# Kernel optimization log

Hardware: AMD Instinct MI355X
Metric: run time of the kernel (lower is better)

The kernel has to match this reference:

```python
import jax, jax.numpy as jnp
import numpy as np
import math

BSZ, SEQ, DM = 2, 2048, 2048
NH, NKV, HD = 16, 8, 128
INTER = 8192
THETA = 10000.0
EPS = 1e-6
SOFTCAP = 50.0


def quant_per_token(x):
    # dynamic per-token symmetric int8 quant: scale = max|x|/127
    s = jnp.max(jnp.abs(x), axis=-1, keepdims=True) / 127.0
    s = jnp.maximum(s, 1e-8)
    q = jnp.clip(jnp.round(x / s), -127.0, 127.0)
    return q, s


def quant_weight(w):
    # per-output-channel symmetric int8 quant (rows are out channels)
    s = jnp.max(jnp.abs(w), axis=1, keepdims=True) / 127.0
    q = jnp.clip(jnp.round(w / s), -127.0, 127.0)
    return q, s


def w8a8_linear(qx, sx, w):
    # int8 GEMM with fused dequant: (qx @ qw^T) * s_act * s_weight
    qw, sw = quant_weight(w)
    return (qx @ qw.T) * sx * sw.T


def rmsnorm_quant(x, w):
    # RMSNormGeneral: w * x / sqrt(mean(x^2)+eps), then per-token quant
    var = jnp.mean(x * x, axis=-1, keepdims=True)
    y = x * jax.lax.rsqrt(var + EPS) * w
    return quant_per_token(y)


def rope_tables(seqlen, dim, theta):
    inv_freq = 1.0 / theta ** (jnp.arange(0, dim, 2, dtype=jnp.float32) / dim)
    pos = jnp.arange(seqlen, dtype=jnp.float32)
    fh = pos[:, None] * inv_freq[None, :]            # [S, dim/2]
    freqs = jnp.concatenate([fh, fh], axis=-1)       # [S, dim]
    return jnp.cos(freqs), jnp.sin(freqs)


def apply_rope(x, cos, sin):
    # x: [B, S, H, D]; rotate-half RoPE
    d2 = x.shape[-1] // 2
    rot = jnp.concatenate([-x[..., d2:], x[..., :d2]], axis=-1)
    return x * cos[None, :, None, :] + rot * sin[None, :, None, :]


def attention(q, k, v, mask, softcap):
    # q: [B, NH, S, D]; k, v: [B, NKV, S, D]
    groups = q.shape[1] // k.shape[1]
    if groups > 1:
        k = jnp.repeat(k, groups, axis=1)
        v = jnp.repeat(v, groups, axis=1)
    scores = jnp.einsum('bhqd,bhkd->bhqk', q, k) / math.sqrt(q.shape[-1])
    if softcap:
        scores = jnp.tanh(scores / softcap) * softcap
    scores = scores + mask
    attn = jax.nn.softmax(scores, axis=-1)
    out = jnp.einsum('bhqk,bhkd->bhqd', attn, v)
    return out.transpose(0, 2, 1, 3).reshape(q.shape[0], q.shape[2], -1)


def setup_inputs() -> dict:
    key = jax.random.key(0)
    ks = jax.random.split(key, 7)
    return {
        'hidden_states': jax.random.normal(ks[0], (BSZ, SEQ, DM), jnp.float32),
        'w_in_norm': jax.random.normal(ks[1], (DM,), jnp.float32) * 0.1 + 1.0,
        'w_post_norm': jax.random.normal(ks[2], (DM,), jnp.float32) * 0.1 + 1.0,
        'wqkv': jax.random.normal(ks[3], (NH * HD + 2 * NKV * HD, DM), jnp.float32) * 0.02,
        'wo': jax.random.normal(ks[4], (DM, NH * HD), jnp.float32) * 0.02,
        'w_gate_up': jax.random.normal(ks[5], (2 * INTER, DM), jnp.float32) * 0.02,
        'w_down': jax.random.normal(ks[6], (DM, INTER), jnp.float32) * 0.02,
    }


def reference(hidden_states, w_in_norm, w_post_norm, wqkv, wo, w_gate_up, w_down):
    q_dim, kv_dim = NH * HD, NKV * HD
    T = BSZ * SEQ
    x = hidden_states.reshape(T, DM)

    # --- attention block ---
    residual = x
    qx, sx = rmsnorm_quant(x, w_in_norm)
    qkv = w8a8_linear(qx, sx, wqkv)                      # [T, q_dim+2*kv_dim]
    q, k, v = jnp.split(qkv, [q_dim, q_dim + kv_dim], axis=-1)
    q = q.reshape(BSZ, SEQ, NH, HD)
    k = k.reshape(BSZ, SEQ, NKV, HD)
    v = v.reshape(BSZ, SEQ, NKV, HD).transpose(0, 2, 1, 3)

    cos, sin = rope_tables(SEQ, HD, THETA)
    q = apply_rope(q, cos, sin).transpose(0, 2, 1, 3)    # [B, NH, S, D]
    k = apply_rope(k, cos, sin).transpose(0, 2, 1, 3)    # [B, NKV, S, D]

    causal = jnp.tril(jnp.ones((SEQ, SEQ), dtype=bool))
    mask = jnp.where(causal, 0.0, -1e9).astype(jnp.float32)[None, None]
    attn_out = attention(q, k, v, mask, SOFTCAP).reshape(T, q_dim)

    qa, sa = quant_per_token(attn_out)
    x = residual + w8a8_linear(qa, sa, wo)

    # --- MLP block ---
    residual = x
    qx, sx = rmsnorm_quant(x, w_post_norm)
    gateup = w8a8_linear(qx, sx, w_gate_up)              # [T, 2*INTER]
    gate, up = jnp.split(gateup, 2, axis=-1)
    act = jax.nn.gelu(gate, approximate=True) * up       # gelu_and_mul
    qm, sm = quant_per_token(act)
    x = residual + w8a8_linear(qm, sm, w_down)

    return x.reshape(BSZ, SEQ, DM)
```

## Files before the change

kernel.cpp:

```cpp
#include <hip/hip_runtime.h>
#include <cstdint>
#include <math.h>

#define T_TOKENS 4096
#define SEQ 2048
#define DM 2048
#define NH 16
#define NKV 8
#define HD 128
#define QDIM 2048
#define KVDIM 1024
#define QKVN 4096
#define INTER 8192
#define GUN 16384

typedef int v4i __attribute__((ext_vector_type(4)));
typedef float v4f __attribute__((ext_vector_type(4)));
typedef short s8v __attribute__((ext_vector_type(8)));
typedef short s4v __attribute__((ext_vector_type(4)));
typedef short s2v __attribute__((ext_vector_type(2)));

#define GL16(g, l)                                                                       \
  __builtin_amdgcn_global_load_lds((__attribute__((address_space(1))) const void*)(g),   \
                                   (__attribute__((address_space(3))) void*)(l), 16, 0, 0)

__device__ inline float wave_sum(float v) {
#pragma unroll
  for (int off = 32; off > 0; off >>= 1) v += __shfl_down(v, off);
  return v;
}
__device__ inline float wave_max(float v) {
#pragma unroll
  for (int off = 32; off > 0; off >>= 1) v = fmaxf(v, __shfl_down(v, off));
  return v;
}
__device__ inline float dot4(float4 a, float4 b) {
  return a.x * b.x + a.y * b.y + a.z * b.z + a.w * b.w;
}
__device__ inline int8_t quant1(float v, float s) {
  float q = rintf(v / s);
  q = fminf(fmaxf(q, -127.f), 127.f);
  return (int8_t)(int)q;
}
__device__ inline unsigned short f2bf_rne(float x) {
  unsigned u = __float_as_uint(x);
  return (unsigned short)((u + 0x7FFFu + ((u >> 16) & 1u)) >> 16);
}
__device__ inline float bf2f(unsigned short h) { return __uint_as_float(((unsigned)h) << 16); }

__global__ void rope_table_kernel(float* __restrict__ cosT, float* __restrict__ sinT) {
  int s = blockIdx.x, d = threadIdx.x;
  float inv = 1.0f / powf(10000.0f, (float)d * (1.0f / 64.0f));
  float f = (float)s * inv;
  cosT[s * 64 + d] = cosf(f);
  sinT[s * 64 + d] = sinf(f);
}

__global__ __launch_bounds__(256) void quant_w_kernel(const float* __restrict__ w,
                                                      int8_t* __restrict__ qw,
                                                      float* __restrict__ sw, int K) {
  __shared__ float red[4];
  int row = blockIdx.x, tid = threadIdx.x;
  const float* wr = w + (size_t)row * K;
  int nv = K >> 10;
  float4 v[8];
  float mx = 0.f;
#pragma unroll
  for (int i = 0; i < 8; i++) {
    if (i < nv) {
      v[i] = *(const float4*)(wr + (size_t)(tid + i * 256) * 4);
      mx = fmaxf(mx, fmaxf(fmaxf(fabsf(v[i].x), fabsf(v[i].y)),
                           fmaxf(fabsf(v[i].z), fabsf(v[i].w))));
    }
  }
  mx = wave_max(mx);
  if ((tid & 63) == 0) red[tid >> 6] = mx;
  __syncthreads();
  float m = fmaxf(fmaxf(red[0], red[1]), fmaxf(red[2], red[3]));
  float s = m * (1.0f / 127.0f);
  if (tid == 0) sw[row] = s;
  float sd = (s > 0.f) ? s : 1.f;
  int8_t* qr = qw + (size_t)row * K;
#pragma unroll
  for (int i = 0; i < 8; i++) {
    if (i < nv) {
      char4 o;
      o.x = quant1(v[i].x, sd);
      o.y = quant1(v[i].y, sd);
      o.z = quant1(v[i].z, sd);
      o.w = quant1(v[i].w, sd);
      *(char4*)(qr + (size_t)(tid + i * 256) * 4) = o;
    }
  }
}

__global__ __launch_bounds__(256) void quant_w_gu_kernel(const float* __restrict__ w,
                                                         int8_t* __restrict__ qw,
                                                         float* __restrict__ sw) {
  __shared__ float red[4];
  int row = blockIdx.x, tid = threadIdx.x;
  const int K = DM;
  int j = (row < INTER) ? row : row - INTER;
  int pr = (j >> 6) * 128 + ((j >> 4) & 3) * 32 + ((row < INTER) ? 0 : 16) + (j & 15);
  const float* wr = w + (size_t)row * K;
  float4 v[2];
  float mx = 0.f;
#pragma unroll
  for (int i = 0; i < 2; i++) {
    v[i] = *(const float4*)(wr + (size_t)(tid + i * 256) * 4);
    mx = fmaxf(mx, fmaxf(fmaxf(fabsf(v[i].x), fabsf(v[i].y)),
                         fmaxf(fabsf(v[i].z), fabsf(v[i].w))));
  }
  mx = wave_max(mx);
  if ((tid & 63) == 0) red[tid >> 6] = mx;
  __syncthreads();
  float m = fmaxf(fmaxf(red[0], red[1]), fmaxf(red[2], red[3]));
  float s = m * (1.0f / 127.0f);
  if (tid == 0) sw[pr] = s;
  float sd = (s > 0.f) ? s : 1.f;
  int8_t* qr = qw + (size_t)pr * K;
#pragma unroll
  for (int i = 0; i < 2; i++) {
    char4 o;
    o.x = quant1(v[i].x, sd);
    o.y = quant1(v[i].y, sd);
    o.z = quant1(v[i].z, sd);
    o.w = quant1(v[i].w, sd);
    *(char4*)(qr + (size_t)(tid + i * 256) * 4) = o;
  }
}

__global__ __launch_bounds__(256) void rmsnorm_quant_kernel(const float* __restrict__ x,
                                                            const float* __restrict__ w,
                                                            int8_t* __restrict__ q,
                                                            float* __restrict__ s) {
  __shared__ float red[8];
  int t = blockIdx.x, tid = threadIdx.x;
  const float* xr = x + (size_t)t * DM;
  float4 a = *(const float4*)(xr + tid * 8);
  float4 b = *(const float4*)(xr + tid * 8 + 4);
  float ss = dot4(a, a) + dot4(b, b);
  ss = wave_sum(ss);
  if ((tid & 63) == 0) red[tid >> 6] = ss;
  __syncthreads();
  float tot = red[0] + red[1] + red[2] + red[3];
  float rms = rsqrtf(tot * (1.0f / DM) + 1e-6f);
  float4 wa = *(const float4*)(w + tid * 8);
  float4 wb = *(const float4*)(w + tid * 8 + 4);
  float y[8] = {a.x * rms * wa.x, a.y * rms * wa.y, a.z * rms * wa.z, a.w * rms * wa.w,
                b.x * rms * wb.x, b.y * rms * wb.y, b.z * rms * wb.z, b.w * rms * wb.w};
  float mx = 0.f;
#pragma unroll
  for (int i = 0; i < 8; i++) mx = fmaxf(mx, fabsf(y[i]));
  mx = wave_max(mx);
  if ((tid & 63) == 0) red[4 + (tid >> 6)] = mx;
  __syncthreads();
  float m = fmaxf(fmaxf(red[4], red[5]), fmaxf(red[6], red[7]));
  float sc = fmaxf(m * (1.0f / 127.0f), 1e-8f);
  if (tid == 0) s[t] = sc;
  int8_t* qr = q + (size_t)t * DM + tid * 8;
  char4 o0, o1;
  o0.x = quant1(y[0], sc); o0.y = quant1(y[1], sc); o0.z = quant1(y[2], sc); o0.w = quant1(y[3], sc);
  o1.x = quant1(y[4], sc); o1.y = quant1(y[5], sc); o1.z = quant1(y[6], sc); o1.w = quant1(y[7], sc);
  *(char4*)(qr) = o0;
  *(char4*)(qr + 4) = o1;
}

__global__ __launch_bounds__(256) void quant_rows_2048_kernel(const float* __restrict__ x,
                                                              int8_t* __restrict__ q,
                                                              float* __restrict__ s) {
  __shared__ float red[4];
  int t = blockIdx.x, tid = threadIdx.x;
  const float* xr = x + (size_t)t * DM;
  float4 a = *(const float4*)(xr + tid * 8);
  float4 b = *(const float4*)(xr + tid * 8 + 4);
  float y[8] = {a.x, a.y, a.z, a.w, b.x, b.y, b.z, b.w};
  float mx = 0.f;
#pragma unroll
  for (int i = 0; i < 8; i++) mx = fmaxf(mx, fabsf(y[i]));
  mx = wave_max(mx);
  if ((tid & 63) == 0) red[tid >> 6] = mx;
  __syncthreads();
  float m = fmaxf(fmaxf(red[0], red[1]), fmaxf(red[2], red[3]));
  float sc = fmaxf(m * (1.0f / 127.0f), 1e-8f);
  if (tid == 0) s[t] = sc;
  int8_t* qr = q + (size_t)t * DM + tid * 8;
  char4 o0, o1;
  o0.x = quant1(y[0], sc); o0.y = quant1(y[1], sc); o0.z = quant1(y[2], sc); o0.w = quant1(y[3], sc);
  o1.x = quant1(y[4], sc); o1.y = quant1(y[5], sc); o1.z = quant1(y[6], sc); o1.w = quant1(y[7], sc);
  *(char4*)(qr) = o0;
  *(char4*)(qr + 4) = o1;
}

__global__ __launch_bounds__(256) void quant_rows_8192_kernel(const float* __restrict__ x,
                                                              int8_t* __restrict__ q,
                                                              float* __restrict__ s) {
  __shared__ float red[4];
  int t = blockIdx.x, tid = threadIdx.x;
  const float* xr = x + (size_t)t * INTER + tid * 32;
  float y[32];
  float mx = 0.f;
#pragma unroll
  for (int i4 = 0; i4 < 32; i4 += 4) {
    float4 v = *(const float4*)(xr + i4);
    y[i4] = v.x; y[i4 + 1] = v.y; y[i4 + 2] = v.z; y[i4 + 3] = v.w;
    mx = fmaxf(mx, fmaxf(fmaxf(fabsf(v.x), fabsf(v.y)), fmaxf(fabsf(v.z), fabsf(v.w))));
  }
  mx = wave_max(mx);
  if ((tid & 63) == 0) red[tid >> 6] = mx;
  __syncthreads();
  float m = fmaxf(fmaxf(red[0], red[1]), fmaxf(red[2], red[3]));
  float sc = fmaxf(m * (1.0f / 127.0f), 1e-8f);
  if (tid == 0) s[t] = sc;
  int8_t* qr = q + (size_t)t * INTER + tid * 32;
#pragma unroll
  for (int i4 = 0; i4 < 32; i4 += 4) {
    char4 o;
    o.x = quant1(y[i4], sc);
    o.y = quant1(y[i4 + 1], sc);
    o.z = quant1(y[i4 + 2], sc);
    o.w = quant1(y[i4 + 3], sc);
    *(char4*)(qr + i4) = o;
  }
}

__global__ __launch_bounds__(256) void cvt_q_kernel(const float* __restrict__ qf,
                                                    const float* __restrict__ cosT,
                                                    const float* __restrict__ sinT,
                                                    unsigned short* __restrict__ Qhi,
                                                    unsigned short* __restrict__ Qlo) {
  int t = blockIdx.x, tid = threadIdx.x;
  int sp = t & (SEQ - 1);
  int h = tid >> 4, pb = (tid & 15) * 4;
  const float* row = qf + (size_t)t * QDIM + h * HD;
  float4 x0 = *(const float4*)(row + pb);
  float4 x1 = *(const float4*)(row + pb + 64);
  float4 c = *(const float4*)(cosT + sp * 64 + pb);
  float4 s = *(const float4*)(sinT + sp * 64 + pb);
  float y0[4] = {x0.x * c.x - x1.x * s.x, x0.y * c.y - x1.y * s.y, x0.z * c.z - x1.z * s.z,
                 x0.w * c.w - x1.w * s.w};
  float y1[4] = {x1.x * c.x + x0.x * s.x, x1.y * c.y + x0.y * s.y, x1.z * c.z + x0.z * s.z,
                 x1.w * c.w + x0.w * s.w};
  s4v h0, l0, h1, l1;
#pragma unroll
  for (int e = 0; e < 4; e++) {
    unsigned short hb = f2bf_rne(y0[e]);
    h0[e] = (short)hb;
    l0[e] = (short)f2bf_rne(y0[e] - bf2f(hb));
    hb = f2bf_rne(y1[e]);
    h1[e] = (short)hb;
    l1[e] = (short)f2bf_rne(y1[e] - bf2f(hb));
  }
  size_t o = (size_t)t * QDIM + h * HD + pb;
  *(s4v*)&Qhi[o] = h0;
  *(s4v*)&Qlo[o] = l0;
  *(s4v*)&Qhi[o + 64] = h1;
  *(s4v*)&Qlo[o + 64] = l1;
}

__global__ __launch_bounds__(256) void cvt_k_kernel(const float* __restrict__ kvf,
                                                    const float* __restrict__ cosT,
                                                    const float* __restrict__ sinT,
                                                    unsigned short* __restrict__ Khi,
                                                    unsigned short* __restrict__ Klo) {
  int t = blockIdx.x, tid = threadIdx.x;
  int sp = t & (SEQ - 1);
  int b = t >> 11;
  int g = tid >> 5, pb = (tid & 31) * 2;
  const float* row = kvf + (size_t)t * DM + g * HD;
  float2 x0 = *(const float2*)(row + pb);
  float2 x1 = *(const float2*)(row + pb + 64);
  float2 c = *(const float2*)(cosT + sp * 64 + pb);
  float2 s = *(const float2*)(sinT + sp * 64 + pb);
  float y0[2] = {x0.x * c.x - x1.x * s.x, x0.y * c.y - x1.y * s.y};
  float y1[2] = {x1.x * c.x + x0.x * s.x, x1.y * c.y + x0.y * s.y};
  s2v h0, l0, h1, l1;
#pragma unroll
  for (int e = 0; e < 2; e++) {
    unsigned short hb = f2bf_rne(y0[e]);
    h0[e] = (short)hb;
    l0[e] = (short)f2bf_rne(y0[e] - bf2f(hb));
    hb = f2bf_rne(y1[e]);
    h1[e] = (short)hb;
    l1[e] = (short)f2bf_rne(y1[e] - bf2f(hb));
  }
  size_t o = ((size_t)(b * NKV + g) * SEQ + sp) * HD + pb;
  *(s2v*)&Khi[o] = h0;
  *(s2v*)&Klo[o] = l0;
  *(s2v*)&Khi[o + 64] = h1;
  *(s2v*)&Klo[o + 64] = l1;
}

__global__ __launch_bounds__(256) void cvt_v_kernel(const float* __restrict__ kvf,
                                                    unsigned short* __restrict__ Vt) {
  __shared__ float vt[32][132];
  int bg = blockIdx.y;
  int b = bg >> 3, g = bg & 7;
  int s0 = blockIdx.x * 32;
  int tid = threadIdx.x;
#pragma unroll
  for (int i = 0; i < 4; i++) {
    int pos = tid + i * 256;
    int r = pos >> 5, d4 = (pos & 31) * 4;
    *(float4*)&vt[r][d4] =
        *(const float4*)(kvf + (size_t)(b * SEQ + s0 + r) * DM + KVDIM + g * HD + d4);
  }
  __syncthreads();
  int d = tid & 127, half = tid >> 7;
  unsigned short u[16];
#pragma unroll
  for (int i = 0; i < 16; i++) u[i] = f2bf_rne(vt[half * 16 + i][d]);
  unsigned short* dst =
      Vt + (size_t)bg * HD * SEQ + (size_t)(s0 >> 5) * 4096 + (half * 2) * 1024 + d * 8;
  *(s8v*)dst = *(s8v*)&u[0];
  *(s8v*)(dst + 1024) = *(s8v*)&u[8];
}

template <int BK>
__global__ __launch_bounds__(256) void gemm_i8_kernel(const int8_t* __restrict__ A,
                                                      const float* __restrict__ sA,
                                                      const int8_t* __restrict__ B,
                                                      const float* __restrict__ sB,
                                                      const float* __restrict__ res,
                                                      float* __restrict__ C, int N, int K) {
  constexpr int NCH = BK / 16;
  constexpr int RS = 4096 / BK;
  constexpr int ISS = BK / 32;
  __shared__ __align__(16) int8_t lA[128 * BK];
  __shared__ __align__(16) int8_t lB[128 * BK];
  int tid = threadIdx.x;
  unsigned nx = gridDim.x;
  unsigned hw = blockIdx.y * nx + blockIdx.x;
  unsigned nwg = nx * gridDim.y;
  unsigned work = (hw & 7) * (nwg >> 3) + (hw >> 3);
  int row0 = (int)(work / nx) * 128;
  int col0 = (int)(work % nx) * 128;
  int lane = tid & 63, wid = tid >> 6;
  int wm = (wid >> 1) * 64, wn = (wid & 1) * 64;
  int fr = lane & 15, lq = lane >> 4;

  int rT = tid / NCH;
  int cT = tid % NCH;
  int colS = ((cT ^ (rT & (NCH - 1))) << 4);
  const int8_t* gA = A + (size_t)(row0 + rT) * K + colS;
  const int8_t* gB = B + (size_t)(col0 + rT) * K + colS;
  int8_t* lAd = &lA[tid * 16];
  int8_t* lBd = &lB[tid * 16];

  int swzk = (fr & (NCH - 1)) << 4;
  int aoff[4], boff[4];
#pragma unroll
  for (int m = 0; m < 4; m++) {
    aoff[m] = (wm + m * 16 + fr) * BK;
    boff[m] = (wn + m * 16 + fr) * BK;
  }

  v4i acc[4][4];
#pragma unroll
  for (int m = 0; m < 4; m++)
#pragma unroll
    for (int n = 0; n < 4; n++) acc[m][n] = (v4i){0, 0, 0, 0};

  for (int k0 = 0; k0 < K; k0 += BK) {
#pragma unroll
    for (int i = 0; i < ISS; i++) GL16(gA + k0 + (size_t)(RS * i) * K, lAd + i * 4096);
#pragma unroll
    for (int i = 0; i < ISS; i++) GL16(gB + k0 + (size_t)(RS * i) * K, lBd + i * 4096);
    __syncthreads();
#pragma unroll
    for (int kk = 0; kk < BK / 64; kk++) {
      int kc = (kk * 64 + lq * 16) ^ swzk;
      v4i a[4], b[4];
#pragma unroll
      for (int m = 0; m < 4; m++) a[m] = *(const v4i*)&lA[aoff[m] + kc];
#pragma unroll
      for (int n = 0; n < 4; n++) b[n] = *(const v4i*)&lB[boff[n] + kc];
#pragma unroll
      for (int m = 0; m < 4; m++)
#pragma unroll
        for (int n = 0; n < 4; n++)
          acc[m][n] = __builtin_amdgcn_mfma_i32_16x16x64_i8(a[m], b[n], acc[m][n], 0, 0, 0);
    }
    __syncthreads();
  }
  int rj = lq * 4;
  int cn = fr;
#pragma unroll
  for (int m = 0; m < 4; m++) {
#pragma unroll
    for (int j = 0; j < 4; j++) {
      int rl = row0 + wm + m * 16 + rj + j;
      float sa = sA[rl];
      size_t rowoff = (size_t)rl * N;
#pragma unroll
      for (int n = 0; n < 4; n++) {
        int cg = col0 + wn + n * 16 + cn;
        float v = (float)acc[m][n][j] * sa * sB[cg];
        if (res) v += res[rowoff + cg];
        C[rowoff + cg] = v;
      }
    }
  }
}

__global__ __launch_bounds__(256) void gemm_gu_fused_kernel(const int8_t* __restrict__ A,
                                                            const float* __restrict__ sA,
                                                            const int8_t* __restrict__ B,
                                                            const float* __restrict__ sB,
                                                            float* __restrict__ act) {
  __shared__ __align__(16) int8_t lA[16384];
  __shared__ __align__(16) int8_t lB[16384];
  const int K = DM;
  int tid = threadIdx.x;
  unsigned nx = gridDim.x;
  unsigned ny = gridDim.y;
  unsigned hw = blockIdx.y * nx + blockIdx.x;
  unsigned nwg = nx * ny;
  unsigned work = (hw & 7) * (nwg >> 3) + (hw >> 3);
  int row0 = (int)(work % ny) * 128;
  int col0 = (int)(work / ny) * 128;
  int lane = tid & 63, wid = tid >> 6;
  int wm = (wid >> 1) * 64, wn = (wid & 1) * 64;
  int fr = lane & 15, lq = lane >> 4;

  int rT = tid >> 3;
  int colS = ((tid & 7) << 4) ^ ((rT & 7) << 4);
  const int8_t* gA = A + (size_t)(row0 + rT) * K + colS;
  const int8_t* gB = B + (size_t)(col0 + rT) * K + colS;
  int8_t* lAd = &lA[tid * 16];
  int8_t* lBd = &lB[tid * 16];

  int swzk = (fr & 7) << 4;
  int aoff[4], boff[4];
#pragma unroll
  for (int m = 0; m < 4; m++) {
    aoff[m] = (wm + m * 16 + fr) * 128;
    boff[m] = (wn + m * 16 + fr) * 128;
  }

  v4i acc[4][4];
#pragma unroll
  for (int m = 0; m < 4; m++)
#pragma unroll
    for (int n = 0; n < 4; n++) acc[m][n] = (v4i){0, 0, 0, 0};

  for (int k0 = 0; k0 < K; k0 += 128) {
#pragma unroll
    for (int i = 0; i < 4; i++) GL16(gA + k0 + (size_t)(32 * i) * K, lAd + i * 4096);
#pragma unroll
    for (int i = 0; i < 4; i++) GL16(gB + k0 + (size_t)(32 * i) * K, lBd + i * 4096);
    __syncthreads();
#pragma unroll
    for (int kk = 0; kk < 2; kk++) {
      int kc = (kk * 64 + lq * 16) ^ swzk;
      v4i a[4], b[4];
#pragma unroll
      for (int m = 0; m < 4; m++) a[m] = *(const v4i*)&lA[aoff[m] + kc];
#pragma unroll
      for (int n = 0; n < 4; n++) b[n] = *(const v4i*)&lB[boff[n] + kc];
#pragma unroll
      for (int m = 0; m < 4; m++)
#pragma unroll
        for (int n = 0; n < 4; n++)
          acc[m][n] = __builtin_amdgcn_mfma_i32_16x16x64_i8(a[m], b[n], acc[m][n], 0, 0, 0);
    }
    __syncthreads();
  }
  int rj = lq * 4;
  int cn = fr;
#pragma unroll
  for (int m = 0; m < 4; m++) {
#pragma unroll
    for (int j = 0; j < 4; j++) {
      int rl = row0 + wm + m * 16 + rj + j;
      float sa = sA[rl];
      size_t rowoff = (size_t)rl * INTER;
#pragma unroll
      for (int np = 0; np < 2; np++) {
        float gv = (float)acc[m][np * 2][j] * sa * sB[col0 + wn + (np * 2) * 16 + cn];
        float uv = (float)acc[m][np * 2 + 1][j] * sa * sB[col0 + wn + (np * 2 + 1) * 16 + cn];
        float inner = 0.7978845608028654f * (gv + 0.044715f * gv * gv * gv);
        float gl = 0.5f * gv * (1.0f + tanhf(inner));
        int jg = (col0 >> 1) + (wn >> 1) + np * 16 + cn;
        act[rowoff + jg] = gl * uv;
      }
    }
  }
}

__global__ __launch_bounds__(256, 2) void attn_mfma_kernel(
    const unsigned short* __restrict__ Qhi, const unsigned short* __restrict__ Qlo,
    const unsigned short* __restrict__ Khi, const unsigned short* __restrict__ Klo,
    const unsigned short* __restrict__ Vt, float* __restrict__ out) {
  __shared__ __align__(16) int8_t lkh[3][8192], lkl[3][8192], lvt[3][8192];
  __shared__ unsigned short ps[4][16][32];
  int hwid = blockIdx.y * gridDim.x + blockIdx.x;
  int work = (hwid & 7) * 64 + (hwid >> 3);
  int bg = work >> 5;
  int rest = work & 31;
  int pi = rest >> 1;
  int hh = rest & 1;
  int qtS = pi, qtL = 31 - pi;
  int b = bg >> 3, g = bg & 7;
  int tid = threadIdx.x;
  int lane = tid & 63, w = tid >> 6;
  int lr = lane & 15, lq = lane >> 4;
  int h = g * 2 + hh;
  int qbS = qtS * 64 + w * 16;
  int qbL = qtL * 64 + w * 16;

  const int8_t* kbh = (const int8_t*)(Khi + (size_t)bg * SEQ * HD);
  const int8_t* kbl = (const int8_t*)(Klo + (size_t)bg * SEQ * HD);
  const int8_t* vb = (const int8_t*)(Vt + (size_t)bg * HD * SEQ);

  int x0 = tid * 16, x1 = x0 + 4096;
  int sK0 = x0 ^ (((x0 >> 8) & 7) << 4);
  int sK1 = x1 ^ (((x1 >> 8) & 7) << 4);

  s8v qhS[4], qlS[4], qhL[4], qlL[4];
  {
    size_t qoS = (size_t)(b * SEQ + qbS + lr) * QDIM + h * HD + lq * 8;
    size_t qoL = (size_t)(b * SEQ + qbL + lr) * QDIM + h * HD + lq * 8;
#pragma unroll
    for (int c = 0; c < 4; ++c) {
      qhS[c] = *(const s8v*)(Qhi + qoS + c * 32);
      qlS[c] = *(const s8v*)(Qlo + qoS + c * 32);
      qhL[c] = *(const s8v*)(Qhi + qoL + c * 32);
      qlL[c] = *(const s8v*)(Qlo + qoL + c * 32);
    }
  }

  v4f oaccS[8], oaccL[8];
#pragma unroll
  for (int i = 0; i < 8; ++i) {
    oaccS[i] = (v4f){0.f, 0.f, 0.f, 0.f};
    oaccL[i] = (v4f){0.f, 0.f, 0.f, 0.f};
  }
  float lsumS[4] = {0.f, 0.f, 0.f, 0.f};
  float lsumL[4] = {0.f, 0.f, 0.f, 0.f};
  const float kin2 = 0.0035355339059327374f;

  int kswz = (lr & 7) << 4;
  int kcol = lq * 16;
  int vbase = lq * 2048 + lr * 16;

  int ktiles = 2 * qtL + 2;

#define STAGE(kt, buf)                                  \
  do {                                                  \
    size_t kb = (size_t)(kt) * 8192;                    \
    GL16(kbh + kb + sK0, &lkh[buf][x0]);                \
    GL16(kbh + kb + sK1, &lkh[buf][x1]);                \
    GL16(kbl + kb + sK0, &lkl[buf][x0]);                \
    GL16(kbl + kb + sK1, &lkl[buf][x1]);                \
    GL16(vb + kb + x0, &lvt[buf][x0]);                  \
    GL16(vb + kb + x1, &lvt[buf][x1]);                  \
  } while (0)

#define TILE_COMPUTE(qb, qh, ql, oacc, lsum)                                           \
  do {                                                                                 \
    v4f sacc[2];                                                                       \
    __builtin_amdgcn_s_setprio(1);                                                     \
    _Pragma("unroll") for (int t2 = 0; t2 < 2; ++t2) {                                 \
      v4f s1 = (v4f){0.f, 0.f, 0.f, 0.f};                                              \
      v4f s2 = (v4f){0.f, 0.f, 0.f, 0.f};                                              \
      v4f s3 = (v4f){0.f, 0.f, 0.f, 0.f};                                              \
      int rowb = (t2 * 16 + lr) * 256;                                                 \
      _Pragma("unroll") for (int c = 0; c < 4; ++c) {                                  \
        int off = rowb + ((c * 64 + kcol) ^ kswz);                                     \
        s8v kh = *(const s8v*)&lkh[cur][off];                                          \
        s8v kl = *(const s8v*)&lkl[cur][off];                                          \
        s1 = __builtin_amdgcn_mfma_f32_16x16x32_bf16(qh[c], kh, s1, 0, 0, 0);          \
        s2 = __builtin_amdgcn_mfma_f32_16x16x32_bf16(qh[c], kl, s2, 0, 0, 0);          \
        s3 = __builtin_amdgcn_mfma_f32_16x16x32_bf16(ql[c], kh, s3, 0, 0, 0);          \
      }                                                                                \
      sacc[t2] = (s1 + s2) + s3;                                                       \
    }                                                                                  \
    __builtin_amdgcn_s_setprio(0);                                                     \
    _Pragma("unroll") for (int j = 0; j < 4; ++j) {                                    \
      int qg = (qb) + lq * 4 + j;                                                      \
      int k0g = kbase + lr, k1g = kbase + 16 + lr;                                     \
      float z0 = __expf(sacc[0][j] * kin2);                                            \
      float z1 = __expf(sacc[1][j] * kin2);                                            \
      float e0 = __expf(-100.f * __builtin_amdgcn_rcpf(z0 + 1.f));                     \
      float e1 = __expf(-100.f * __builtin_amdgcn_rcpf(z1 + 1.f));                     \
      e0 = (k0g <= qg) ? e0 : 0.f;                                                     \
      e1 = (k1g <= qg) ? e1 : 0.f;                                                     \
      lsum[j] += e0 + e1;                                                              \
      int q = lq * 4 + j;                                                              \
      ps[w][q][lr] = f2bf_rne(e0);                                                     \
      ps[w][q][16 + lr] = f2bf_rne(e1);                                                \
    }                                                                                  \
    s8v pa = *(const s8v*)&ps[w][lr][lq * 8];                                          \
    __builtin_amdgcn_s_setprio(1);                                                     \
    _Pragma("unroll") for (int dt = 0; dt < 8; ++dt) {                                 \
      s8v vh = *(const s8v*)&lvt[cur][vbase + dt * 256];                               \
      oacc[dt] = __builtin_amdgcn_mfma_f32_16x16x32_bf16(pa, vh, oacc[dt], 0, 0, 0);   \
    }                                                                                  \
    __builtin_amdgcn_s_setprio(0);                                                     \
  } while (0)

  STAGE(0, 0);
  STAGE(1, 1);
  int cur = 0;
  for (int kt = 0; kt < ktiles; ++kt) {
    if (kt + 1 < ktiles) {
      asm volatile("s_waitcnt vmcnt(6)" ::: "memory");
    } else {
      asm volatile("s_waitcnt vmcnt(0)" ::: "memory");
    }
    __builtin_amdgcn_s_barrier();
    __builtin_amdgcn_sched_barrier(0);
    int stg = cur + 2;
    if (stg >= 3) stg -= 3;
    if (kt + 2 < ktiles) STAGE(kt + 2, stg);
    int kbase = kt * 32;
    TILE_COMPUTE(qbL, qhL, qlL, oaccL, lsumL);
    if (kbase <= qbS + 15) TILE_COMPUTE(qbS, qhS, qlS, oaccS, lsumS);
    cur = (cur == 2) ? 0 : cur + 1;
  }
#undef TILE_COMPUTE
#undef STAGE

#pragma unroll
  for (int st = 1; st <= 8; st <<= 1)
#pragma unroll
    for (int j = 0; j < 4; ++j) {
      lsumS[j] += __shfl_xor(lsumS[j], st);
      lsumL[j] += __shfl_xor(lsumL[j], st);
    }

  float invS[4], invL[4];
#pragma unroll
  for (int j = 0; j < 4; ++j) {
    invS[j] = 1.f / lsumS[j];
    invL[j] = 1.f / lsumL[j];
  }
  float* obS = out + (size_t)(b * SEQ + qbS) * QDIM + h * HD;
  float* obL = out + (size_t)(b * SEQ + qbL) * QDIM + h * HD;
#pragma unroll
  for (int dt = 0; dt < 8; ++dt)
#pragma unroll
    for (int j = 0; j < 4; ++j) {
      obS[(size_t)(lq * 4 + j) * QDIM + dt * 16 + lr] = oaccS[dt][j] * invS[j];
      obL[(size_t)(lq * 4 + j) * QDIM + dt * 16 + lr] = oaccL[dt][j] * invL[j];
    }
}

extern "C" void kernel_launch(void* const* d_in, const int* in_sizes, int n_in, void* d_out,
                              int out_size, void* d_ws, size_t ws_size, hipStream_t stream) {
  (void)in_sizes; (void)n_in; (void)out_size; (void)ws_size;
  const float* hidden = (const float*)d_in[0];
  const float* w_in_norm = (const float*)d_in[1];
  const float* w_post_norm = (const float*)d_in[2];
  const float* wqkv = (const float*)d_in[3];
  const float* wo = (const float*)d_in[4];
  const float* w_gate_up = (const float*)d_in[5];
  const float* w_down = (const float*)d_in[6];
  float* out = (float*)d_out;

  char* p = (char*)d_ws;
  size_t off = 0;
  auto take = [&](size_t bytes) -> char* {
    char* r = p + off;
    off += (bytes + 255) & ~(size_t)255;
    return r;
  };
  const size_t MB = 1u << 20;
  int8_t* qx = (int8_t*)take((size_t)T_TOKENS * DM);
  float* sx = (float*)take((size_t)T_TOKENS * 4);
  int8_t* qw_qkv = (int8_t*)take((size_t)QKVN * DM);
  float* sw_qkv = (float*)take((size_t)QKVN * 4);
  int8_t* qw_wo = (int8_t*)take((size_t)DM * QDIM);
  float* sw_wo = (float*)take((size_t)DM * 4);
  int8_t* qw_gu = (int8_t*)take((size_t)GUN * DM);
  float* sw_gu = (float*)take((size_t)GUN * 4);
  int8_t* qw_dn = (int8_t*)take((size_t)DM * INTER);
  float* sw_dn = (float*)take((size_t)DM * 4);
  float* cosT = (float*)take((size_t)SEQ * 64 * 4);
  float* sinT = (float*)take((size_t)SEQ * 64 * 4);
  float* x1 = (float*)take((size_t)T_TOKENS * DM * 4);
  float* s_act = (float*)take((size_t)T_TOKENS * 4);
  char* regB = take(96 * MB);
  float* qf32 = (float*)regB;
  float* kvf32 = (float*)regB;
  float* attn_out = (float*)regB;
  unsigned short* Qhi = (unsigned short*)(regB + 32 * MB);
  unsigned short* Qlo = (unsigned short*)(regB + 48 * MB);
  unsigned short* Khi = (unsigned short*)(regB + 64 * MB);
  unsigned short* Klo = (unsigned short*)(regB + 72 * MB);
  unsigned short* Vt = (unsigned short*)(regB + 80 * MB);
  float* act_f32 = (float*)regB;
  int8_t* act_q8 = (int8_t*)(regB + 64 * MB);

  rope_table_kernel<<<SEQ, 64, 0, stream>>>(cosT, sinT);
  quant_w_kernel<<<QKVN, 256, 0, stream>>>(wqkv, qw_qkv, sw_qkv, DM);
  quant_w_kernel<<<DM, 256, 0, stream>>>(wo, qw_wo, sw_wo, QDIM);
  quant_w_gu_kernel<<<GUN, 256, 0, stream>>>(w_gate_up, qw_gu, sw_gu);
  quant_w_kernel<<<DM, 256, 0, stream>>>(w_down, qw_dn, sw_dn, INTER);

  rmsnorm_quant_kernel<<<T_TOKENS, 256, 0, stream>>>(hidden, w_in_norm, qx, sx);
  gemm_i8_kernel<256><<<dim3(QDIM / 128, T_TOKENS / 128), 256, 0, stream>>>(
      qx, sx, qw_qkv, sw_qkv, nullptr, qf32, QDIM, DM);
  cvt_q_kernel<<<T_TOKENS, 256, 0, stream>>>(qf32, cosT, sinT, Qhi, Qlo);
  gemm_i8_kernel<256><<<dim3(DM / 128, T_TOKENS / 128), 256, 0, stream>>>(
      qx, sx, qw_qkv + (size_t)QDIM * DM, sw_qkv + QDIM, nullptr, kvf32, DM, DM);
  cvt_k_kernel<<<T_TOKENS, 256, 0, stream>>>(kvf32, cosT, sinT, Khi, Klo);
  cvt_v_kernel<<<dim3(SEQ / 32, 16), 256, 0, stream>>>(kvf32, Vt);
  attn_mfma_kernel<<<dim3(32, 16), 256, 0, stream>>>(Qhi, Qlo, Khi, Klo, Vt, attn_out);
  quant_rows_2048_kernel<<<T_TOKENS, 256, 0, stream>>>(attn_out, qx, sx);
  gemm_i8_kernel<256><<<dim3(DM / 128, T_TOKENS / 128), 256, 0, stream>>>(
      qx, sx, qw_wo, sw_wo, hidden, x1, DM, QDIM);

  rmsnorm_quant_kernel<<<T_TOKENS, 256, 0, stream>>>(x1, w_post_norm, qx, sx);
  for (int ch = 0; ch < 4; ++ch) {
    const int8_t* qxc = qx + (size_t)ch * 1024 * DM;
    const float* sxc = sx + (size_t)ch * 1024;
    gemm_gu_fused_kernel<<<dim3(GUN / 128, 1024 / 128), 256, 0, stream>>>(qxc, sxc, qw_gu, sw_gu,
                                                                          act_f32);
    quant_rows_8192_kernel<<<1024, 256, 0, stream>>>(act_f32, act_q8 + (size_t)ch * 1024 * INTER,
                                                     s_act + (size_t)ch * 1024);
  }
  gemm_i8_kernel<256><<<dim3(DM / 128, T_TOKENS / 128), 256, 0, stream>>>(
      act_q8, s_act, qw_dn, sw_dn, x1, out, DM, INTER);
}
```

Measured before the change: 670.1 us.

## Double-buffer LDS tiles in int8 GEMM kernels to overlap loads with MFMA

Both int8 GEMM kernels now keep two LDS buffers of 128-wide K tiles. The next tile is prefetched with global_load_lds while MFMAs run on the current one, and a single waitcnt plus barrier replaces the two __syncthreads per iteration. The generic kernel drops its BK=256 template and uses BK=128 with double buffering, so total LDS stays at 64KB. This hides global-load latency, at the cost of more barriers per K step and possibly lower occupancy in the fused gate-up kernel, whose LDS use doubles.

```diff
diff --git a/kernel.cpp b/kernel.cpp
--- a/kernel.cpp
+++ b/kernel.cpp
@@ -316,18 +316,14 @@
   *(s8v*)(dst + 1024) = *(s8v*)&u[8];
 }
 
-template <int BK>
 __global__ __launch_bounds__(256) void gemm_i8_kernel(const int8_t* __restrict__ A,
                                                       const float* __restrict__ sA,
                                                       const int8_t* __restrict__ B,
                                                       const float* __restrict__ sB,
                                                       const float* __restrict__ res,
                                                       float* __restrict__ C, int N, int K) {
-  constexpr int NCH = BK / 16;
-  constexpr int RS = 4096 / BK;
-  constexpr int ISS = BK / 32;
-  __shared__ __align__(16) int8_t lA[128 * BK];
-  __shared__ __align__(16) int8_t lB[128 * BK];
+  __shared__ __align__(16) int8_t lA[2][16384];
+  __shared__ __align__(16) int8_t lB[2][16384];
   int tid = threadIdx.x;
   unsigned nx = gridDim.x;
   unsigned hw = blockIdx.y * nx + blockIdx.x;
@@ -339,20 +335,17 @@
   int wm = (wid >> 1) * 64, wn = (wid & 1) * 64;
   int fr = lane & 15, lq = lane >> 4;
 
-  int rT = tid / NCH;
-  int cT = tid % NCH;
-  int colS = ((cT ^ (rT & (NCH - 1))) << 4);
+  int rT = tid >> 3;
+  int colS = ((tid & 7) << 4) ^ ((rT & 7) << 4);
   const int8_t* gA = A + (size_t)(row0 + rT) * K + colS;
   const int8_t* gB = B + (size_t)(col0 + rT) * K + colS;
-  int8_t* lAd = &lA[tid * 16];
-  int8_t* lBd = &lB[tid * 16];
-
-  int swzk = (fr & (NCH - 1)) << 4;
+
+  int swzk = (fr & 7) << 4;
   int aoff[4], boff[4];
 #pragma unroll
   for (int m = 0; m < 4; m++) {
-    aoff[m] = (wm + m * 16 + fr) * BK;
-    boff[m] = (wn + m * 16 + fr) * BK;
+    aoff[m] = (wm + m * 16 + fr) * 128;
+    boff[m] = (wn + m * 16 + fr) * 128;
   }
 
   v4i acc[4][4];
@@ -361,28 +354,45 @@
 #pragma unroll
     for (int n = 0; n < 4; n++) acc[m][n] = (v4i){0, 0, 0, 0};
 
-  for (int k0 = 0; k0 < K; k0 += BK) {
-#pragma unroll
-    for (int i = 0; i < ISS; i++) GL16(gA + k0 + (size_t)(RS * i) * K, lAd + i * 4096);
-#pragma unroll
-    for (int i = 0; i < ISS; i++) GL16(gB + k0 + (size_t)(RS * i) * K, lBd + i * 4096);
-    __syncthreads();
-#pragma unroll
-    for (int kk = 0; kk < BK / 64; kk++) {
+#define GSTAGE(t, buf)                                                           \
+  do {                                                                           \
+    int kk0 = (t) * 128;                                                         \
+    _Pragma("unroll") for (int i = 0; i < 4; i++) {                              \
+      GL16(gA + kk0 + (size_t)(32 * i) * K, &lA[buf][tid * 16 + i * 4096]);      \
+      GL16(gB + kk0 + (size_t)(32 * i) * K, &lB[buf][tid * 16 + i * 4096]);      \
+    }                                                                            \
+  } while (0)
+
+  int nt = K >> 7;
+  GSTAGE(0, 0);
+  asm volatile("s_waitcnt vmcnt(0)" ::: "memory");
+  __builtin_amdgcn_s_barrier();
+  __builtin_amdgcn_sched_barrier(0);
+  int cur = 0;
+  for (int t = 0; t < nt; ++t) {
+    if (t + 1 < nt) GSTAGE(t + 1, cur ^ 1);
+#pragma unroll
+    for (int kk = 0; kk < 2; kk++) {
       int kc = (kk * 64 + lq * 16) ^ swzk;
       v4i a[4], b[4];
 #pragma unroll
-      for (int m = 0; m < 4; m++) a[m] = *(const v4i*)&lA[aoff[m] + kc];
-#pragma unroll
-      for (int n = 0; n < 4; n++) b[n] = *(const v4i*)&lB[boff[n] + kc];
+      for (int m = 0; m < 4; m++) a[m] = *(const v4i*)&lA[cur][aoff[m] + kc];
+#pragma unroll
+      for (int n = 0; n < 4; n++) b[n] = *(const v4i*)&lB[cur][boff[n] + kc];
 #pragma unroll
       for (int m = 0; m < 4; m++)
 #pragma unroll
         for (int n = 0; n < 4; n++)
           acc[m][n] = __builtin_amdgcn_mfma_i32_16x16x64_i8(a[m], b[n], acc[m][n], 0, 0, 0);
     }
-    __syncthreads();
-  }
+    if (t + 1 < nt) {
+      asm volatile("s_waitcnt vmcnt(0)" ::: "memory");
+      __builtin_amdgcn_s_barrier();
+      __builtin_amdgcn_sched_barrier(0);
+      cur ^= 1;
+    }
+  }
+#undef GSTAGE
   int rj = lq * 4;
   int cn = fr;
 #pragma unroll
@@ -408,8 +418,8 @@
                                                             const int8_t* __restrict__ B,
                                                             const float* __restrict__ sB,
                                                             float* __restrict__ act) {
-  __shared__ __align__(16) int8_t lA[16384];
-  __shared__ __align__(16) int8_t lB[16384];
+  __shared__ __align__(16) int8_t lA[2][16384];
+  __shared__ __align__(16) int8_t lB[2][16384];
   const int K = DM;
   int tid = threadIdx.x;
   unsigned nx = gridDim.x;
@@ -427,8 +437,6 @@
   int colS = ((tid & 7) << 4) ^ ((rT & 7) << 4);
   const int8_t* gA = A + (size_t)(row0 + rT) * K + colS;
   const int8_t* gB = B + (size_t)(col0 + rT) * K + colS;
-  int8_t* lAd = &lA[tid * 16];
-  int8_t* lBd = &lB[tid * 16];
 
   int swzk = (fr & 7) << 4;
   int aoff[4], boff[4];
@@ -444,28 +452,45 @@
 #pragma unroll
     for (int n = 0; n < 4; n++) acc[m][n] = (v4i){0, 0, 0, 0};
 
-  for (int k0 = 0; k0 < K; k0 += 128) {
-#pragma unroll
-    for (int i = 0; i < 4; i++) GL16(gA + k0 + (size_t)(32 * i) * K, lAd + i * 4096);
-#pragma unroll
-    for (int i = 0; i < 4; i++) GL16(gB + k0 + (size_t)(32 * i) * K, lBd + i * 4096);
-    __syncthreads();
+#define GSTAGE(t, buf)                                                           \
+  do {                                                                           \
+    int kk0 = (t) * 128;                                                         \
+    _Pragma("unroll") for (int i = 0; i < 4; i++) {                              \
+      GL16(gA + kk0 + (size_t)(32 * i) * K, &lA[buf][tid * 16 + i * 4096]);      \
+      GL16(gB + kk0 + (size_t)(32 * i) * K, &lB[buf][tid * 16 + i * 4096]);      \
+    }                                                                            \
+  } while (0)
+
+  const int nt = K >> 7;
+  GSTAGE(0, 0);
+  asm volatile("s_waitcnt vmcnt(0)" ::: "memory");
+  __builtin_amdgcn_s_barrier();
+  __builtin_amdgcn_sched_barrier(0);
+  int cur = 0;
+  for (int t = 0; t < nt; ++t) {
+    if (t + 1 < nt) GSTAGE(t + 1, cur ^ 1);
 #pragma unroll
     for (int kk = 0; kk < 2; kk++) {
       int kc = (kk * 64 + lq * 16) ^ swzk;
       v4i a[4], b[4];
 #pragma unroll
-      for (int m = 0; m < 4; m++) a[m] = *(const v4i*)&lA[aoff[m] + kc];
-#pragma unroll
-      for (int n = 0; n < 4; n++) b[n] = *(const v4i*)&lB[boff[n] + kc];
+      for (int m = 0; m < 4; m++) a[m] = *(const v4i*)&lA[cur][aoff[m] + kc];
+#pragma unroll
+      for (int n = 0; n < 4; n++) b[n] = *(const v4i*)&lB[cur][boff[n] + kc];
 #pragma unroll
       for (int m = 0; m < 4; m++)
 #pragma unroll
         for (int n = 0; n < 4; n++)
           acc[m][n] = __builtin_amdgcn_mfma_i32_16x16x64_i8(a[m], b[n], acc[m][n], 0, 0, 0);
     }
-    __syncthreads();
-  }
+    if (t + 1 < nt) {
+      asm volatile("s_waitcnt vmcnt(0)" ::: "memory");
+      __builtin_amdgcn_s_barrier();
+      __builtin_amdgcn_sched_barrier(0);
+      cur ^= 1;
+    }
+  }
+#undef GSTAGE
   int rj = lq * 4;
   int cn = fr;
 #pragma unroll
@@ -700,16 +725,16 @@
   quant_w_kernel<<<DM, 256, 0, stream>>>(w_down, qw_dn, sw_dn, INTER);
 
   rmsnorm_quant_kernel<<<T_TOKENS, 256, 0, stream>>>(hidden, w_in_norm, qx, sx);
-  gemm_i8_kernel<256><<<dim3(QDIM / 128, T_TOKENS / 128), 256, 0, stream>>>(
+  gemm_i8_kernel<<<dim3(QDIM / 128, T_TOKENS / 128), 256, 0, stream>>>(
       qx, sx, qw_qkv, sw_qkv, nullptr, qf32, QDIM, DM);
   cvt_q_kernel<<<T_TOKENS, 256, 0, stream>>>(qf32, cosT, sinT, Qhi, Qlo);
-  gemm_i8_kernel<256><<<dim3(DM / 128, T_TOKENS / 128), 256, 0, stream>>>(
+  gemm_i8_kernel<<<dim3(DM / 128, T_TOKENS / 128), 256, 0, stream>>>(
       qx, sx, qw_qkv + (size_t)QDIM * DM, sw_qkv + QDIM, nullptr, kvf32, DM, DM);
   cvt_k_kernel<<<T_TOKENS, 256, 0, stream>>>(kvf32, cosT, sinT, Khi, Klo);
   cvt_v_kernel<<<dim3(SEQ / 32, 16), 256, 0, stream>>>(kvf32, Vt);
   attn_mfma_kernel<<<dim3(32, 16), 256, 0, stream>>>(Qhi, Qlo, Khi, Klo, Vt, attn_out);
   quant_rows_2048_kernel<<<T_TOKENS, 256, 0, stream>>>(attn_out, qx, sx);
-  gemm_i8_kernel<256><<<dim3(DM / 128, T_TOKENS / 128), 256, 0, stream>>>(
+  gemm_i8_kernel<<<dim3(DM / 128, T_TOKENS / 128), 256, 0, stream>>>(
       qx, sx, qw_wo, sw_wo, hidden, x1, DM, QDIM);
 
   rmsnorm_quant_kernel<<<T_TOKENS, 256, 0, stream>>>(x1, w_post_norm, qx, sx);
@@ -721,6 +746,6 @@
     quant_rows_8192_kernel<<<1024, 256, 0, stream>>>(act_f32, act_q8 + (size_t)ch * 1024 * INTER,
                                                      s_act + (size_t)ch * 1024);
   }
-  gemm_i8_kernel<256><<<dim3(DM / 128, T_TOKENS / 128), 256, 0, stream>>>(
+  gemm_i8_kernel<<<dim3(DM / 128, T_TOKENS / 128), 256, 0, stream>>>(
       act_q8, s_act, qw_dn, sw_dn, x1, out, DM, INTER);
 }
```

Result: slower. 688.1 us (+2.7%).
